# Kernel optimization log

Hardware: AMD Instinct MI355X
Metric: run time of the kernel (lower is better)

## Reference

```python
import jax, jax.numpy as jnp
import numpy as np

N_HEAD, D_HEAD = 16, 64
D_MODEL = N_HEAD * D_HEAD
QLEN, MLEN, BSZ = 1024, 1024, 4
KLEN = QLEN + MLEN
LN_EPS = 1e-5


def setup_inputs() -> dict:
    key = jax.random.key(0)
    ks = jax.random.split(key, 8)
    w = jax.random.normal(ks[0], (QLEN, BSZ, D_MODEL), jnp.float32)
    r = jax.random.normal(ks[1], (KLEN, D_MODEL), jnp.float32)
    mems = jax.random.normal(ks[2], (MLEN, BSZ, D_MODEL), jnp.float32)
    # causal mask over (qlen, klen): query i may attend keys j <= i + MLEN
    i = jnp.arange(QLEN)[:, None]
    j = jnp.arange(KLEN)[None, :]
    attn_mask = j > (i + MLEN)  # True = masked
    s = 1.0 / np.sqrt(D_MODEL)
    qkv_w = jax.random.normal(ks[3], (3 * D_MODEL, D_MODEL), jnp.float32) * s
    r_net_w = jax.random.normal(ks[4], (D_MODEL, D_MODEL), jnp.float32) * s
    o_w = jax.random.normal(ks[5], (D_MODEL, D_MODEL), jnp.float32) * s
    r_r_bias = jax.random.normal(ks[6], (N_HEAD, D_HEAD), jnp.float32) * 0.02
    r_w_bias = jax.random.normal(ks[7], (N_HEAD, D_HEAD), jnp.float32) * 0.02
    ln_gamma = jnp.ones((D_MODEL,), jnp.float32)
    ln_beta = jnp.zeros((D_MODEL,), jnp.float32)
    return {"w": w, "r": r, "mems": mems, "attn_mask": attn_mask,
            "qkv_w": qkv_w, "r_net_w": r_net_w, "o_w": o_w,
            "r_r_bias": r_r_bias, "r_w_bias": r_w_bias,
            "ln_gamma": ln_gamma, "ln_beta": ln_beta}


def _layer_norm(x, g, b):
    mu = jnp.mean(x, axis=-1, keepdims=True)
    var = jnp.var(x, axis=-1, keepdims=True)
    return (x - mu) * jax.lax.rsqrt(var + LN_EPS) * g + b


def _rel_shift(x):
    # x: [qlen, rlen, bsz, n_head]
    q, rl, b, n = x.shape
    x_pad = jnp.pad(x, ((0, 0), (1, 0), (0, 0), (0, 0)))  # zero row at front of axis 1
    x_pad = x_pad.reshape(rl + 1, q, b, n)
    return x_pad[1:].reshape(q, rl, b, n)


def reference(w, r, mems, attn_mask, qkv_w, r_net_w, o_w, r_r_bias, r_w_bias, ln_gamma, ln_beta):
    qlen, bsz = w.shape[0], w.shape[1]
    cat = jnp.concatenate([mems, w], axis=0)  # [klen, b, d]
    klen = cat.shape[0]
    w_heads = cat @ qkv_w.T  # [klen, b, 3*d]
    r_head_k = (r @ r_net_w.T).reshape(r.shape[0], N_HEAD, D_HEAD)  # [rlen, n, dh]
    w_q, w_k, w_v = jnp.split(w_heads, 3, axis=-1)
    w_q = w_q[-qlen:].reshape(qlen, bsz, N_HEAD, D_HEAD)
    w_k = w_k.reshape(klen, bsz, N_HEAD, D_HEAD)
    w_v = w_v.reshape(klen, bsz, N_HEAD, D_HEAD)

    scale = 1.0 / np.sqrt(D_HEAD)
    AC = jnp.einsum('ibnd,jbnd->ijbn', w_q + r_w_bias, w_k)
    BD = _rel_shift(jnp.einsum('ibnd,jnd->ijbn', w_q + r_r_bias, r_head_k))
    attn_score = (AC + BD) * scale
    attn_score = jnp.where(attn_mask[None, :, :, None].transpose(1, 2, 0, 3), -1e30, attn_score) if False else \
        jnp.where(attn_mask[:, :, None, None], jnp.float32(-1e30), attn_score)
    attn_prob = jax.nn.softmax(attn_score, axis=1)
    attn_vec = jnp.einsum('ijbn,jbnd->ibnd', attn_prob, w_v)
    attn_vec = attn_vec.reshape(qlen, bsz, N_HEAD * D_HEAD)
    attn_out = attn_vec @ o_w.T
    return _layer_norm(w + attn_out, ln_gamma, ln_beta)
```

## Files before the change

### kernel.cpp

```cpp
#include <hip/hip_runtime.h>
#include <hip/hip_bf16.h>

typedef __attribute__((ext_vector_type(8))) short short8;
typedef __attribute__((ext_vector_type(4))) float f32x4;
typedef __hip_bfloat16 bf16;

#define NHEAD 16
#define DHEAD 64
#define DMODEL 1024
#define QLEN 1024
#define MLEN 1024
#define BSZ 4
#define KLEN 2048
#define LOG2E 1.44269504088896f

__device__ __forceinline__ float fast_exp2(float x) {
#if __has_builtin(__builtin_amdgcn_exp2f)
  return __builtin_amdgcn_exp2f(x);
#else
  return exp2f(x);
#endif
}

__device__ __forceinline__ short8 ld8(const bf16* p) { return *(const short8*)p; }
__device__ __forceinline__ void st8(bf16* p, short8 v) { *(short8*)p = v; }
__device__ __forceinline__ f32x4 mfma16(short8 a, short8 b, f32x4 c) {
  return __builtin_amdgcn_mfma_f32_16x16x32_bf16(a, b, c, 0, 0, 0);
}
__device__ __forceinline__ float bfu2f(unsigned short u) {
  unsigned int x = ((unsigned int)u) << 16;
  return __uint_as_float(x);
}
__device__ __forceinline__ unsigned short f2bfu(float f) {
  bf16 t = __float2bfloat16(f);
  return *(unsigned short*)&t;
}
__device__ __forceinline__ unsigned short f2bfu_fast(float f) {
  return (unsigned short)((__float_as_uint(f) + 0x8000u) >> 16);
}
__device__ __forceinline__ bf16 bf16_raw(unsigned short u) {
  bf16 t; *(unsigned short*)&t = u; return t;
}
__device__ __forceinline__ void async16(const bf16* g, bf16* l) {
  __builtin_amdgcn_global_load_lds(
      (const __attribute__((address_space(1))) unsigned int*)g,
      (__attribute__((address_space(3))) unsigned int*)l, 16, 0, 0);
}

#define DPPF(x, ctrl, rm) \
  __int_as_float(__builtin_amdgcn_update_dpp( \
      __float_as_int(x), __float_as_int(x), (ctrl), (rm), 0xF, false))

__global__ void detect_dtype(const unsigned short* wq, int* flag) {
  const int tid = threadIdx.x;
  int cnt = 0;
  #pragma unroll
  for (int j = 0; j < 8; ++j) {
    unsigned short u = wq[2 * (tid * 8 + j)];
    int e = (u >> 7) & 0xFF;
    if (e >= 100 && e <= 134) cnt++;
  }
  #pragma unroll
  for (int o = 32; o > 0; o >>= 1) cnt += __shfl_xor(cnt, o, 64);
  __shared__ int red[4];
  if ((tid & 63) == 0) red[tid >> 6] = cnt;
  __syncthreads();
  if (tid == 0) {
    int total = red[0] + red[1] + red[2] + red[3];
    *flag = (total > 1024) ? 0 : 1;
  }
}

__global__ __launch_bounds__(256) void convert_inputs(
    const void* s0, const void* s1, const void* s2,
    const void* s3, const void* s4, const void* s5,
    bf16* d0, bf16* d1, bf16* d2, bf16* d3, bf16* d4, bf16* d5,
    const int* flag)
{
  const int b = blockIdx.x;
  const void* src; bf16* dst; int lb;
  if (b < 2048)      { src = s0; dst = d0; lb = b; }
  else if (b < 4096) { src = s1; dst = d1; lb = b - 2048; }
  else if (b < 5120) { src = s2; dst = d2; lb = b - 4096; }
  else if (b < 6656) { src = s3; dst = d3; lb = b - 5120; }
  else if (b < 7168) { src = s4; dst = d4; lb = b - 6656; }
  else               { src = s5; dst = d5; lb = b - 7168; }
  const size_t idx = ((size_t)lb * 256 + threadIdx.x) * 8;
  if (*flag) {
    const f32x4* f = (const f32x4*)src;
    f32x4 a = f[idx >> 2];
    f32x4 c = f[(idx >> 2) + 1];
    short8 v;
    v[0] = (short)f2bfu(a[0]); v[1] = (short)f2bfu(a[1]);
    v[2] = (short)f2bfu(a[2]); v[3] = (short)f2bfu(a[3]);
    v[4] = (short)f2bfu(c[0]); v[5] = (short)f2bfu(c[1]);
    v[6] = (short)f2bfu(c[2]); v[7] = (short)f2bfu(c[3]);
    st8(dst + idx, v);
  } else {
    st8(dst + idx, ld8((const bf16*)src + idx));
  }
}

__device__ __forceinline__ void gemm_core64(
    const bf16* const ap[4], const bf16* const bp[4],
    bf16* As, bf16* Bs, int wv, int wm, int wn, int lr, int lg,
    f32x4 acc[4][4])
{
  const int sx = lr & 7;
  for (int k0 = 0; k0 < DMODEL; k0 += 64) {
    #pragma unroll
    for (int p = 0; p < 4; ++p) {
      async16(ap[p] + k0, As + (wv * 32 + p * 8) * 64);
      async16(bp[p] + k0, Bs + (wv * 32 + p * 8) * 64);
    }
    __syncthreads();
    #pragma unroll
    for (int ks = 0; ks < 2; ++ks) {
      const int col = (((ks * 4 + lg) ^ sx) << 3);
      short8 af[4], bfr[4];
      #pragma unroll
      for (int mt = 0; mt < 4; ++mt) af[mt] = ld8(As + (wm * 64 + mt * 16 + lr) * 64 + col);
      #pragma unroll
      for (int nt = 0; nt < 4; ++nt) bfr[nt] = ld8(Bs + (wn * 64 + nt * 16 + lr) * 64 + col);
      #pragma unroll
      for (int mt = 0; mt < 4; ++mt)
        #pragma unroll
        for (int nt = 0; nt < 4; ++nt)
          acc[mt][nt] = mfma16(af[mt], bfr[nt], acc[mt][nt]);
    }
    __syncthreads();
  }
}

__global__ __launch_bounds__(256) void qkv_gemm(
    const bf16* __restrict__ w, const bf16* __restrict__ mems,
    const bf16* __restrict__ qkv_w,
    const bf16* __restrict__ r, const bf16* __restrict__ rnet_w,
    const void* __restrict__ r_w_bias, const void* __restrict__ r_r_bias,
    const int* __restrict__ flag,
    bf16* __restrict__ qac, bf16* __restrict__ qbd,
    bf16* __restrict__ kbuf, bf16* __restrict__ vbuf,
    bf16* __restrict__ rkbuf)
{
  const int id = blockIdx.x;
  int sec, bx, by;
  if (id < 256)       { sec = 0; bx = id >> 5;                    by = 32 + (id & 31); }
  else if (id < 768)  { sec = 1; int t = id - 256;  bx = 8  + (t >> 6); by = t & 63; }
  else if (id < 1280) { sec = 2; int t = id - 768;  bx = 16 + (t >> 6); by = t & 63; }
  else                { sec = 3; int t = id - 1280; bx = 24 + (t >> 4); by = t & 15; }
  __shared__ bf16 sh[16384];
  bf16* As = sh;
  bf16* Bs = sh + 8192;
  const int tid = threadIdx.x;
  const int lane = tid & 63, wv = tid >> 6;
  const int wm = wv >> 1, wn = wv & 1;
  const int lr = lane & 15, lg = lane >> 4;
  const int lr8 = lane >> 3;
  const int ucol = ((lane & 7) ^ lr8) * 8;
  const bf16 *ap[4], *bp[4];
  #pragma unroll
  for (int p = 0; p < 4; ++p) {
    int arow = wv * 32 + p * 8 + lr8;
    if (sec == 3) {
      ap[p] = r + (size_t)(by * 128 + arow) * DMODEL + ucol;
      bp[p] = rnet_w + (size_t)((bx - 24) * 128 + arow) * DMODEL + ucol;
    } else {
      int m = by * 128 + arow;
      int j = m >> 2, b = m & 3;
      ap[p] = ((j < MLEN) ? (mems + ((size_t)(j * BSZ + b)) * DMODEL)
                          : (w + ((size_t)((j - MLEN) * BSZ + b)) * DMODEL)) + ucol;
      bp[p] = qkv_w + (size_t)(bx * 128 + arow) * DMODEL + ucol;
    }
  }
  f32x4 zero = {0.f, 0.f, 0.f, 0.f};
  f32x4 acc[4][4];
  #pragma unroll
  for (int a = 0; a < 4; ++a)
    #pragma unroll
    for (int c2 = 0; c2 < 4; ++c2) acc[a][c2] = zero;
  gemm_core64(ap, bp, As, Bs, wv, wm, wn, lr, lg, acc);

  if (sec == 2) {
    #pragma unroll
    for (int nt = 0; nt < 4; ++nt) {
      int n = wn * 64 + nt * 16 + lr;
      #pragma unroll
      for (int mt = 0; mt < 4; ++mt) {
        int jl = wm * 16 + mt * 4 + lg;
        #pragma unroll
        for (int rr = 0; rr < 4; ++rr) {
          int x = rr * 32 + jl;
          sh[n * 128 + (((x >> 4) ^ (n & 7)) << 4) + (x & 15)] =
              __float2bfloat16(acc[mt][nt][rr]);
        }
      }
    }
    __syncthreads();
    const int grp = lane >> 3, sl = lane & 7;
    const int hbase = (bx - 16) * 2;
    #pragma unroll
    for (int i = 0; i < 16; ++i) {
      int idx = i * 32 + wv * 8 + grp;
      int n = idx >> 2, bb = idx & 3;
      int x0 = bb * 32 + sl * 4;
      ushort4 v4 = *(const ushort4*)(sh + n * 128 + (((x0 >> 4) ^ (n & 7)) << 4) + (x0 & 15));
      int hh = hbase + (n >> 6), dd = n & 63;
      *(ushort4*)(vbuf + ((size_t)(bb * NHEAD + hh) * DHEAD + dd) * KLEN + by * 32 + sl * 4) = v4;
    }
    return;
  }
  if (sec == 3) {
    #pragma unroll
    for (int nt = 0; nt < 4; ++nt) {
      int col = (bx - 24) * 128 + wn * 64 + nt * 16 + lr;
      int h = col >> 6, d = col & 63;
      #pragma unroll
      for (int mt = 0; mt < 4; ++mt) {
        #pragma unroll
        for (int rr = 0; rr < 4; ++rr) {
          int m = by * 128 + wm * 64 + mt * 16 + lg * 4 + rr;
          rkbuf[((size_t)h * KLEN + m) * DHEAD + d] = __float2bfloat16(acc[mt][nt][rr]);
        }
      }
    }
    return;
  }
  const int isf = (sec == 0) ? *flag : 0;
  const float QSC = 0.125f * LOG2E;
  #pragma unroll
  for (int nt = 0; nt < 4; ++nt) {
    int col = bx * 128 + wn * 64 + nt * 16 + lr;
    int nn = col & 1023;
    int h = nn >> 6, d = nn & 63;
    float rwb = 0.f, rrb = 0.f;
    if (sec == 0) {
      if (isf) { rwb = ((const float*)r_w_bias)[nn]; rrb = ((const float*)r_r_bias)[nn]; }
      else { rwb = __bfloat162float(((const bf16*)r_w_bias)[nn]);
             rrb = __bfloat162float(((const bf16*)r_r_bias)[nn]); }
    }
    #pragma unroll
    for (int mt = 0; mt < 4; ++mt) {
      #pragma unroll
      for (int rr = 0; rr < 4; ++rr) {
        int m = by * 128 + wm * 64 + mt * 16 + lg * 4 + rr;
        int j = m >> 2, b = m & 3;
        float v = acc[mt][nt][rr];
        if (sec == 0) {
          int i = j - MLEN;
          size_t base = (((size_t)(b * NHEAD + h)) * QLEN + i) * DHEAD + d;
          qac[base] = __float2bfloat16((v + rwb) * QSC);
          qbd[base] = __float2bfloat16((v + rrb) * QSC);
        } else {
          kbuf[(((size_t)(b * NHEAD + h)) * KLEN + j) * DHEAD + d] = __float2bfloat16(v);
        }
      }
    }
  }
}

#define RRBODY(RR, CTRL) { \
    const int di = g * 4 + RR; \
    float sh[5]; \
    _Pragma("unroll") for (int ct = 0; ct < 5; ++ct) { \
      float y = Gr[ct][RR]; \
      sh[ct] = __int_as_float(__builtin_amdgcn_update_dpp( \
          __float_as_int(y), __float_as_int(y), (CTRL), 0xF, 0xF, false)); \
    } \
    float sv[4]; \
    _Pragma("unroll") for (int jt = 0; jt < 4; ++jt) { \
      float bd = (c > di) ? sh[jt + 1] : sh[jt]; \
      sv[jt] = S[jt][RR] + bd; \
    } \
    if (lastt) { \
      const int ig = i0 + wv * 16 + di; \
      _Pragma("unroll") for (int jt = 0; jt < 4; ++jt) \
        if (j0 + jt * 16 + c > ig + MLEN) sv[jt] = -1e30f; \
    } \
    _Pragma("unroll") for (int jt = 0; jt < 4; ++jt) { \
      float pv = fast_exp2(sv[jt]); \
      ls[RR] += pv; \
      pw[di * 64 + ((((jt * 2) + (c >> 3)) ^ (di & 7)) << 3) + (c & 7)] = \
          bf16_raw(f2bfu_fast(pv)); \
    } \
  }

__global__ __launch_bounds__(256, 4) void attn_kernel(
    const bf16* __restrict__ qac, const bf16* __restrict__ qbd,
    const bf16* __restrict__ kbuf, const bf16* __restrict__ vbuf,
    const bf16* __restrict__ rkbuf, bf16* __restrict__ av)
{
  const int id = blockIdx.x;
  const int qt = 15 - (id >> 6);
  const int bh = id & 63;
  const int b = bh >> 4, h = bh & 15;
  const int i0 = qt * 64;
  __shared__ bf16 Ks[64 * 64];
  __shared__ bf16 Vt[64 * 64];
  __shared__ bf16 Rs[128 * 64];
  __shared__ bf16 Ps[4 * 16 * 64];
  const int tid = threadIdx.x;
  const int wv = tid >> 6, lane = tid & 63;
  const int c = lane & 15, g = lane >> 4;
  const size_t bhb = (size_t)(b * NHEAD + h);
  const int lr8 = lane >> 3;
  const int ucol = ((lane & 7) ^ lr8) * 8;
  const int sw0 = ((0 + g) ^ (c & 7)) * 8;
  const int sw1 = ((4 + g) ^ (c & 7)) * 8;

  short8 qaf[2], qbf[2];
  {
    const size_t qrow = (bhb * QLEN + i0 + wv * 16 + c) * DHEAD;
    #pragma unroll
    for (int ks = 0; ks < 2; ++ks) {
      qaf[ks] = ld8(qac + qrow + ks * 32 + g * 8);
      qbf[ks] = ld8(qbd + qrow + ks * 32 + g * 8);
    }
  }
  f32x4 zero = {0.f, 0.f, 0.f, 0.f};
  f32x4 O[4];
  #pragma unroll
  for (int dt = 0; dt < 4; ++dt) O[dt] = zero;
  float ls[4] = {0.f, 0.f, 0.f, 0.f};

  bf16* pw = Ps + wv * (16 * 64);
  const bf16* kc = Ks + c * 64;
  const bf16* vc = Vt + c * 64;
  const int relb = c + 48 - wv * 16;
  int relo[2][5];
  #pragma unroll
  for (int ks = 0; ks < 2; ++ks)
    #pragma unroll
    for (int ct = 0; ct < 5; ++ct)
      relo[ks][ct] = (relb + ct * 16) * 64 + (ks ? sw1 : sw0);

  const int ntiles = qt + 17;
  int roff = ((15 - qt) & 1) << 6;
  for (int t = 0; t < ntiles; ++t) {
    const int j0 = t * 64;
    const int m_lo = j0 - i0 + 960;
    const int ro = roff << 6;
    #pragma unroll
    for (int p = 0; p < 2; ++p) {
      int r0 = wv * 16 + p * 8;
      async16(kbuf + (bhb * KLEN + j0 + r0 + lr8) * DHEAD + ucol, Ks + r0 * 64);
      async16(vbuf + (bhb * DHEAD + r0 + lr8) * KLEN + j0 + ucol, Vt + r0 * 64);
    }
    if (t == 0) {
      #pragma unroll
      for (int p = 0; p < 4; ++p) {
        int r0 = wv * 32 + p * 8;
        async16(rkbuf + ((size_t)h * KLEN + m_lo + r0 + lr8) * DHEAD + ucol,
                Rs + ((r0 << 6) ^ ro));
      }
      asm volatile("s_waitcnt vmcnt(4)" ::: "memory");
    } else {
      #pragma unroll
      for (int p = 0; p < 2; ++p) {
        int r1 = 64 + wv * 16 + p * 8;
        async16(rkbuf + ((size_t)h * KLEN + m_lo + r1 + lr8) * DHEAD + ucol,
                Rs + ((r1 << 6) ^ ro));
      }
      asm volatile("s_waitcnt vmcnt(2)" ::: "memory");
    }
    __builtin_amdgcn_s_barrier();
    __builtin_amdgcn_sched_barrier(0);
    f32x4 S[4], G[5];
    #pragma unroll
    for (int jt = 0; jt < 4; ++jt) S[jt] = zero;
    #pragma unroll
    for (int ct = 0; ct < 5; ++ct) G[ct] = zero;
    #pragma unroll
    for (int ks = 0; ks < 2; ++ks) {
      const int sw = ks ? sw1 : sw0;
      #pragma unroll
      for (int jt = 0; jt < 4; ++jt)
        S[jt] = mfma16(qaf[ks], ld8(kc + jt * 1024 + sw), S[jt]);
    }
    __builtin_amdgcn_sched_barrier(0);
    asm volatile("s_waitcnt vmcnt(0)" ::: "memory");
    __syncthreads();
    #pragma unroll
    for (int ks = 0; ks < 2; ++ks) {
      #pragma unroll
      for (int ct = 0; ct < 5; ++ct)
        G[ct] = mfma16(qbf[ks], ld8(Rs + (relo[ks][ct] ^ ro)), G[ct]);
    }
    float Gr[5][4];
    #pragma unroll
    for (int ct = 0; ct < 5; ++ct)
      #pragma unroll
      for (int rr = 0; rr < 4; ++rr) {
        float y = G[ct][rr];
        y = DPPF(y, 0x124, 0xA);
        y = DPPF(y, 0x128, 0xC);
        Gr[ct][rr] = y;
      }
    const bool lastt = (t == ntiles - 1);
    RRBODY(0, 0x121)
    RRBODY(1, 0x122)
    RRBODY(2, 0x123)
    RRBODY(3, 0x124)
    #pragma unroll
    for (int ks = 0; ks < 2; ++ks) {
      short8 pf = ld8(pw + c * 64 + (((ks * 4 + g) ^ (c & 7)) << 3));
      const int sw = ks ? sw1 : sw0;
      #pragma unroll
      for (int dt = 0; dt < 4; ++dt)
        O[dt] = mfma16(pf, ld8(vc + dt * 1024 + sw), O[dt]);
    }
    __syncthreads();
    roff ^= 64;
  }
  #pragma unroll
  for (int rr = 0; rr < 4; ++rr) {
    float s = ls[rr];
    s += DPPF(s, 0xB1, 0xF);
    s += DPPF(s, 0x4E, 0xF);
    s += DPPF(s, 0x141, 0xF);
    s += DPPF(s, 0x140, 0xF);
    ls[rr] = s;
  }
  #pragma unroll
  for (int rr = 0; rr < 4; ++rr) {
    float inv = 1.0f / ls[rr];
    #pragma unroll
    for (int dt = 0; dt < 4; ++dt) {
      int ig = i0 + wv * 16 + g * 4 + rr;
      int d = dt * 16 + c;
      av[((size_t)ig * BSZ + b) * DMODEL + h * DHEAD + d] =
          __float2bfloat16(O[dt][rr] * inv);
    }
  }
}

__global__ __launch_bounds__(256) void out_gemm(
    const bf16* __restrict__ av, const bf16* __restrict__ o_w,
    bf16* __restrict__ ao)
{
  const int id = blockIdx.x;
  const int bx = id >> 5, by = id & 31;
  __shared__ bf16 As[128 * 64];
  __shared__ bf16 Bs[128 * 64];
  const int tid = threadIdx.x;
  const int lane = tid & 63, wv = tid >> 6;
  const int wm = wv >> 1, wn = wv & 1;
  const int lr = lane & 15, lg = lane >> 4;
  const int lr8 = lane >> 3;
  const int ucol = ((lane & 7) ^ lr8) * 8;
  const bf16 *ap[4], *bp[4];
  #pragma unroll
  for (int p = 0; p < 4; ++p) {
    int arow = wv * 32 + p * 8 + lr8;
    ap[p] = av + (size_t)(by * 128 + arow) * DMODEL + ucol;
    bp[p] = o_w + (size_t)(bx * 128 + arow) * DMODEL + ucol;
  }
  f32x4 zero = {0.f, 0.f, 0.f, 0.f};
  f32x4 acc[4][4];
  #pragma unroll
  for (int a = 0; a < 4; ++a)
    #pragma unroll
    for (int c2 = 0; c2 < 4; ++c2) acc[a][c2] = zero;
  gemm_core64(ap, bp, As, Bs, wv, wm, wn, lr, lg, acc);
  #pragma unroll
  for (int nt = 0; nt < 4; ++nt) {
    int col = bx * 128 + wn * 64 + nt * 16 + lr;
    #pragma unroll
    for (int mt = 0; mt < 4; ++mt) {
      #pragma unroll
      for (int rr = 0; rr < 4; ++rr) {
        int m = by * 128 + wm * 64 + mt * 16 + lg * 4 + rr;
        ao[(size_t)m * DMODEL + col] = __float2bfloat16(acc[mt][nt][rr]);
      }
    }
  }
}

__global__ __launch_bounds__(256) void ln_kernel(
    const void* __restrict__ wz, const bf16* __restrict__ ao,
    const void* __restrict__ gz, const void* __restrict__ bz,
    void* __restrict__ outz, const int* __restrict__ flag)
{
  const int m = blockIdx.x;
  const int tid = threadIdx.x;
  const int isf = *flag;
  ushort4 au = ((const ushort4*)ao)[m * 256 + tid];
  float a4[4];
  a4[0] = bfu2f(au.x); a4[1] = bfu2f(au.y); a4[2] = bfu2f(au.z); a4[3] = bfu2f(au.w);
  float x[4], gg[4], bb[4];
  if (isf) {
    f32x4 w4 = ((const f32x4*)wz)[m * 256 + tid];
    f32x4 g4 = ((const f32x4*)gz)[tid];
    f32x4 b4 = ((const f32x4*)bz)[tid];
    #pragma unroll
    for (int k = 0; k < 4; ++k) { x[k] = w4[k] + a4[k]; gg[k] = g4[k]; bb[k] = b4[k]; }
  } else {
    ushort4 w4 = ((const ushort4*)wz)[m * 256 + tid];
    ushort4 g4 = ((const ushort4*)gz)[tid];
    ushort4 b4 = ((const ushort4*)bz)[tid];
    x[0] = bfu2f(w4.x) + a4[0]; x[1] = bfu2f(w4.y) + a4[1];
    x[2] = bfu2f(w4.z) + a4[2]; x[3] = bfu2f(w4.w) + a4[3];
    gg[0] = bfu2f(g4.x); gg[1] = bfu2f(g4.y); gg[2] = bfu2f(g4.z); gg[3] = bfu2f(g4.w);
    bb[0] = bfu2f(b4.x); bb[1] = bfu2f(b4.y); bb[2] = bfu2f(b4.z); bb[3] = bfu2f(b4.w);
  }
  float s = x[0] + x[1] + x[2] + x[3];
  float s2 = x[0]*x[0] + x[1]*x[1] + x[2]*x[2] + x[3]*x[3];
  #pragma unroll
  for (int o = 32; o > 0; o >>= 1) {
    s += __shfl_xor(s, o, 64);
    s2 += __shfl_xor(s2, o, 64);
  }
  __shared__ float red[8];
  const int wv = tid >> 6, lane = tid & 63;
  if (lane == 0) { red[wv] = s; red[4 + wv] = s2; }
  __syncthreads();
  s = red[0] + red[1] + red[2] + red[3];
  s2 = red[4] + red[5] + red[6] + red[7];
  const float mu = s * (1.0f / DMODEL);
  const float var = s2 * (1.0f / DMODEL) - mu * mu;
  const float rstd = rsqrtf(var + 1e-5f);
  float y[4];
  #pragma unroll
  for (int k = 0; k < 4; ++k) y[k] = (x[k] - mu) * rstd * gg[k] + bb[k];
  if (isf) {
    f32x4 o4; o4[0] = y[0]; o4[1] = y[1]; o4[2] = y[2]; o4[3] = y[3];
    ((f32x4*)outz)[m * 256 + tid] = o4;
  } else {
    ushort4 o4;
    o4.x = f2bfu(y[0]); o4.y = f2bfu(y[1]); o4.z = f2bfu(y[2]); o4.w = f2bfu(y[3]);
    ((ushort4*)outz)[m * 256 + tid] = o4;
  }
}

extern "C" void kernel_launch(void* const* d_in, const int* in_sizes, int n_in,
                              void* d_out, int out_size, void* d_ws, size_t ws_size,
                              hipStream_t stream) {
  (void)in_sizes; (void)n_in; (void)out_size; (void)ws_size;
  const void* w      = d_in[0];
  const void* r      = d_in[1];
  const void* mems   = d_in[2];
  const void* qkv_w  = d_in[4];
  const void* rnet_w = d_in[5];
  const void* o_w    = d_in[6];
  const void* rrb    = d_in[7];
  const void* rwb    = d_in[8];
  const void* ln_g   = d_in[9];
  const void* ln_b   = d_in[10];

  char* ws = (char*)d_ws;
  const size_t MB = 1ull << 20;
  bf16* cw    = (bf16*)(ws + 0 * MB);
  bf16* cmems = (bf16*)(ws + 8 * MB);
  bf16* cr    = (bf16*)(ws + 16 * MB);
  bf16* cqkvw = (bf16*)(ws + 20 * MB);
  bf16* crnet = (bf16*)(ws + 26 * MB);
  bf16* cow   = (bf16*)(ws + 28 * MB);
  int*  flag  = (int*)(ws + 30 * MB);
  bf16* qac   = (bf16*)(ws + 31 * MB);
  bf16* qbd   = (bf16*)(ws + 39 * MB);
  bf16* kbuf  = (bf16*)(ws + 47 * MB);
  bf16* vbuf  = (bf16*)(ws + 63 * MB);
  bf16* rkbuf = (bf16*)(ws + 79 * MB);
  bf16* av    = (bf16*)(ws + 83 * MB);
  bf16* ao    = (bf16*)(ws + 0 * MB);

  detect_dtype<<<1, 256, 0, stream>>>((const unsigned short*)w, flag);
  convert_inputs<<<7680, 256, 0, stream>>>(w, mems, r, qkv_w, rnet_w, o_w,
                                           cw, cmems, cr, cqkvw, crnet, cow, flag);
  qkv_gemm<<<1408, 256, 0, stream>>>(cw, cmems, cqkvw, cr, crnet,
                                     rwb, rrb, flag,
                                     qac, qbd, kbuf, vbuf, rkbuf);
  attn_kernel<<<1024, 256, 0, stream>>>(qac, qbd, kbuf, vbuf, rkbuf, av);
  out_gemm<<<256, 256, 0, stream>>>(av, cow, ao);
  ln_kernel<<<dim3(4096), 256, 0, stream>>>(w, ao, ln_g, ln_b, d_out, flag);
}
```

Baseline: 299.9 us.

## Triple-buffer R tiles and prefetch next K/V/R tiles across iterations

Replaces the double-buffered rel-pos key tile with a 3-bank ring buffer and moves the K, V and R async loads to the end of the previous iteration, so the next tile's data arrives while the current tile is finishing. This removes the mid-loop vmcnt(0) wait and extra __syncthreads between the AC and BD MFMAs, letting both score products run back to back. It costs extra LDS (one more 64x64 R bank), which may lower occupancy, and it relies on careful waitcnt accounting for correctness.

New measurement: 296.1 us. Within noise of the previous version (-1.3%).

```diff
diff --git a/kernel.cpp b/kernel.cpp
--- a/kernel.cpp
+++ b/kernel.cpp
@@ -296,7 +296,7 @@
   const int i0 = qt * 64;
   __shared__ bf16 Ks[64 * 64];
   __shared__ bf16 Vt[64 * 64];
-  __shared__ bf16 Rs[128 * 64];
+  __shared__ bf16 Rs[192 * 64];
   __shared__ bf16 Ps[4 * 16 * 64];
   const int tid = threadIdx.x;
   const int wv = tid >> 6, lane = tid & 63;
@@ -325,65 +325,75 @@
   bf16* pw = Ps + wv * (16 * 64);
   const bf16* kc = Ks + c * 64;
   const bf16* vc = Vt + c * 64;
+
   const int relb = c + 48 - wv * 16;
-  int relo[2][5];
+  int loSw[2][5];
   #pragma unroll
   for (int ks = 0; ks < 2; ++ks)
     #pragma unroll
-    for (int ct = 0; ct < 5; ++ct)
-      relo[ks][ct] = (relb + ct * 16) * 64 + (ks ? sw1 : sw0);
+    for (int ct = 0; ct < 5; ++ct) {
+      int rel = relb + ct * 16;
+      loSw[ks][ct] = (rel & 63) * 64 + (ks ? sw1 : sw0);
+    }
 
   const int ntiles = qt + 17;
-  int roff = ((15 - qt) & 1) << 6;
+  const int mlo0 = 960 - i0;
+  const int mb0 = (mlo0 >> 6) % 3;
+  const bf16* rkh = rkbuf + (size_t)h * KLEN * DHEAD;
+
+  #pragma unroll
+  for (int p = 0; p < 2; ++p) {
+    int r0 = wv * 16 + p * 8;
+    async16(kbuf + (bhb * KLEN + r0 + lr8) * DHEAD + ucol, Ks + r0 * 64);
+    async16(vbuf + (bhb * DHEAD + r0 + lr8) * KLEN + ucol, Vt + r0 * 64);
+  }
+  #pragma unroll
+  for (int p = 0; p < 4; ++p) {
+    int rr = wv * 32 + p * 8;
+    int bank = ((rr >> 6) ? ((mb0 + 1) % 3) : mb0) * 4096;
+    async16(rkh + (size_t)(mlo0 + rr + lr8) * DHEAD + ucol,
+            Rs + bank + (rr & 63) * 64);
+  }
+  {
+    const int bank2 = ((mb0 + 2) % 3) * 4096;
+    #pragma unroll
+    for (int p = 0; p < 2; ++p) {
+      int rw = wv * 16 + p * 8;
+      async16(rkh + (size_t)(mlo0 + 128 + rw + lr8) * DHEAD + ucol,
+              Rs + bank2 + rw * 64);
+    }
+  }
+
+  int b0e = mb0 * 4096;
+  int b1e = ((mb0 + 1) % 3) * 4096;
+
   for (int t = 0; t < ntiles; ++t) {
     const int j0 = t * 64;
-    const int m_lo = j0 - i0 + 960;
-    const int ro = roff << 6;
-    #pragma unroll
-    for (int p = 0; p < 2; ++p) {
-      int r0 = wv * 16 + p * 8;
-      async16(kbuf + (bhb * KLEN + j0 + r0 + lr8) * DHEAD + ucol, Ks + r0 * 64);
-      async16(vbuf + (bhb * DHEAD + r0 + lr8) * KLEN + j0 + ucol, Vt + r0 * 64);
-    }
-    if (t == 0) {
-      #pragma unroll
-      for (int p = 0; p < 4; ++p) {
-        int r0 = wv * 32 + p * 8;
-        async16(rkbuf + ((size_t)h * KLEN + m_lo + r0 + lr8) * DHEAD + ucol,
-                Rs + ((r0 << 6) ^ ro));
-      }
-      asm volatile("s_waitcnt vmcnt(4)" ::: "memory");
+    const int m_lo = mlo0 + j0;
+    if (t + 1 < ntiles) {
+      asm volatile("s_waitcnt vmcnt(2)" ::: "memory");
     } else {
-      #pragma unroll
-      for (int p = 0; p < 2; ++p) {
-        int r1 = 64 + wv * 16 + p * 8;
-        async16(rkbuf + ((size_t)h * KLEN + m_lo + r1 + lr8) * DHEAD + ucol,
-                Rs + ((r1 << 6) ^ ro));
-      }
-      asm volatile("s_waitcnt vmcnt(2)" ::: "memory");
+      asm volatile("s_waitcnt vmcnt(0)" ::: "memory");
     }
     __builtin_amdgcn_s_barrier();
     __builtin_amdgcn_sched_barrier(0);
+
     f32x4 S[4], G[5];
     #pragma unroll
     for (int jt = 0; jt < 4; ++jt) S[jt] = zero;
     #pragma unroll
     for (int ct = 0; ct < 5; ++ct) G[ct] = zero;
+    const bf16* rb0 = Rs + b0e;
+    const bf16* rb1 = Rs + b1e;
     #pragma unroll
     for (int ks = 0; ks < 2; ++ks) {
       const int sw = ks ? sw1 : sw0;
       #pragma unroll
       for (int jt = 0; jt < 4; ++jt)
         S[jt] = mfma16(qaf[ks], ld8(kc + jt * 1024 + sw), S[jt]);
-    }
-    __builtin_amdgcn_sched_barrier(0);
-    asm volatile("s_waitcnt vmcnt(0)" ::: "memory");
-    __syncthreads();
-    #pragma unroll
-    for (int ks = 0; ks < 2; ++ks) {
       #pragma unroll
       for (int ct = 0; ct < 5; ++ct)
-        G[ct] = mfma16(qbf[ks], ld8(Rs + (relo[ks][ct] ^ ro)), G[ct]);
+        G[ct] = mfma16(qbf[ks], ld8((ct > wv ? rb1 : rb0) + loSw[ks][ct]), G[ct]);
     }
     float Gr[5][4];
     #pragma unroll
@@ -408,8 +418,28 @@
       for (int dt = 0; dt < 4; ++dt)
         O[dt] = mfma16(pf, ld8(vc + dt * 1024 + sw), O[dt]);
     }
-    __syncthreads();
-    roff ^= 64;
+    asm volatile("s_waitcnt lgkmcnt(0)" ::: "memory");
+    __builtin_amdgcn_s_barrier();
+    __builtin_amdgcn_sched_barrier(0);
+    if (t + 1 < ntiles) {
+      const int j1 = j0 + 64;
+      #pragma unroll
+      for (int p = 0; p < 2; ++p) {
+        int r0 = wv * 16 + p * 8;
+        async16(kbuf + (bhb * KLEN + j1 + r0 + lr8) * DHEAD + ucol, Ks + r0 * 64);
+        async16(vbuf + (bhb * DHEAD + r0 + lr8) * KLEN + j1 + ucol, Vt + r0 * 64);
+      }
+    }
+    if (t + 2 < ntiles) {
+      #pragma unroll
+      for (int p = 0; p < 2; ++p) {
+        int rw = wv * 16 + p * 8;
+        async16(rkh + (size_t)(m_lo + 192 + rw + lr8) * DHEAD + ucol,
+                Rs + b0e + rw * 64);
+      }
+    }
+    int nb = b1e + 4096; if (nb == 12288) nb = 0;
+    b0e = b1e; b1e = nb;
   }
   #pragma unroll
   for (int rr = 0; rr < 4; ++rr) {
```
